# Performance work log

Hardware: AMD Instinct MI355X
Metric: run time of the kernel (lower is better)

The kernel has to match this reference:

```python
import jax, jax.numpy as jnp
import numpy as np

TOL = 1e-3


def _image_grads(F):
    # replicate-pad central difference, matches GradientBatch (conv with [-0.5,0,0.5])
    Fx = jnp.pad(F, ((0, 0), (0, 0), (0, 0), (1, 1)), mode='edge')
    gx = 0.5 * (Fx[:, :, :, 2:] - Fx[:, :, :, :-2])
    Fy = jnp.pad(F, ((0, 0), (0, 0), (1, 1), (0, 0)), mode='edge')
    gy = 0.5 * (Fy[:, :, 2:, :] - Fy[:, :, :-2, :])
    return gx, gy


def _param_to_H(p):
    B = p.shape[0]
    z = jnp.zeros((B, 1, 1), p.dtype)
    return jnp.concatenate([p, z], 1).reshape(B, 3, 3) + jnp.eye(3, dtype=p.dtype)


def _bilinear_sample(A, xw, yw):
    # grid_sample(mode='bilinear', align_corners=True, padding_mode='zeros') at pixel coords (xw, yw)
    B, k, h, w = A.shape
    x0 = jnp.floor(xw)
    y0 = jnp.floor(yw)
    fx = (xw - x0).reshape(B, 1, h * w)
    fy = (yw - y0).reshape(B, 1, h * w)
    Af = A.reshape(B, k, h * w)

    def gather(xi, yi):
        valid = (xi >= 0) & (xi <= w - 1) & (yi >= 0) & (yi <= h - 1)
        xi_c = jnp.clip(xi, 0, w - 1).astype(jnp.int32)
        yi_c = jnp.clip(yi, 0, h - 1).astype(jnp.int32)
        idx = (yi_c * w + xi_c).reshape(B, 1, h * w)
        v = jnp.take_along_axis(Af, jnp.broadcast_to(idx, (B, k, h * w)), axis=2)
        return v * valid.reshape(B, 1, h * w).astype(A.dtype)

    v00 = gather(x0, y0)
    v01 = gather(x0 + 1, y0)
    v10 = gather(x0, y0 + 1)
    v11 = gather(x0 + 1, y0 + 1)
    Q = ((1 - fx) * (1 - fy) * v00 + fx * (1 - fy) * v01
         + (1 - fx) * fy * v10 + fx * fy * v11)
    return Q.reshape(B, k, h, w)


def _deeplk(img, temp, init_param, max_itr):
    B, k, h, w = temp.shape
    dt = temp.dtype
    gx, gy = _image_grads(temp)
    # centered pixel grid (meshgrid in source: x - x.max()/2)
    x = jnp.arange(w, dtype=dt) - (w - 1) / 2.0
    y = jnp.arange(h, dtype=dt) - (h - 1) / 2.0
    X, Y = jnp.meshgrid(x, y)  # (h, w); X varies along w
    Xf = jnp.tile(X.reshape(-1), k)  # [k*h*w], tiled per channel
    Yf = jnp.tile(Y.reshape(-1), k)
    gxf = gx.reshape(B, k * h * w)
    gyf = gy.reshape(B, k * h * w)
    dIdp = jnp.stack([
        Xf * gxf, Yf * gxf, gxf,
        Xf * gyf, Yf * gyf, gyf,
        -Xf * Xf * gxf - Xf * Yf * gyf,
        -Xf * Yf * gxf - Yf * Yf * gyf,
    ], axis=2)  # [B, k*h*w, 8]
    Hmat = jnp.einsum('bnp,bnq->bpq', dIdp, dIdp)  # [B,8,8]
    invH = jnp.linalg.inv(Hmat)
    invH_dIdp = jnp.einsum('bpq,bnq->bpn', invH, dIdp)  # [B,8,k*h*w]
    xy = jnp.stack([X.reshape(-1), Y.reshape(-1), jnp.ones((h * w,), dt)], 0)  # [3, h*w]
    tolf = jnp.asarray(TOL, dt)

    def step(carry, _):
        p, dp = carry
        Hm = _param_to_H(p)
        xyw = jnp.einsum('bij,jn->bin', Hm, xy)  # [B,3,h*w]
        Xw = (xyw[:, 0] / xyw[:, 2]).reshape(B, h, w) + (w - 1) / 2.0
        Yw = (xyw[:, 1] / xyw[:, 2]).reshape(B, h, w) + (h - 1) / 2.0
        Fi_warp = _bilinear_sample(img, Xw, Yw)
        xn = Xw / ((w - 1) / 2.0) - 1.0
        yn = Yw / ((h - 1) / 2.0) - 1.0
        mask = ((xn > -1 + 2.0 / w) & (xn < 1 - 2.0 / w)
                & (yn > -1 + 2.0 / h) & (yn < 1 - 2.0 / h)).astype(dt)
        r = (Fi_warp - temp * mask[:, None]).reshape(B, k * h * w, 1)
        dp_new = jnp.einsum('bpn,bnj->bpj', invH_dIdp, r)  # [B,8,1]
        dp_new = dp_new.at[:, 6:8, 0].set(0.0)  # zero projective terms
        active = (jnp.linalg.norm(dp, axis=1, keepdims=True) > tolf).astype(dt)
        dp2 = active * dp_new  # converged samples freeze (dp stays 0)
        return (p - dp2, dp2), None

    dp0 = jnp.ones((B, 8, 1), dt)
    (p, _), _ = jax.lax.scan(step, (init_param, dp0), None, length=max_itr)
    return p


def setup_inputs() -> dict:
    key = jax.random.key(0)
    k1, k2 = jax.random.split(key)
    B, k, h, w = 8, 8, 256, 256
    img = jax.random.normal(k1, (B, k, h, w), dtype=jnp.float32)
    temp = jax.random.normal(k2, (B, k, h, w), dtype=jnp.float32)
    init_param = jnp.zeros((B, 8, 1), dtype=jnp.float32)
    return {"img": img, "temp": temp, "init_param": init_param, "max_itr": 10}


def reference(img, temp, init_param, max_itr):
    p = _deeplk(img, temp, init_param, max_itr)
    return (p, _param_to_H(p))
```

## Files before the change

kernel.cpp:

```cpp
#include <hip/hip_runtime.h>
#include <hip/hip_bf16.h>

#define B_ 8
#define K_ 8
#define H_ 256
#define W_ 256
#define HW (H_*W_)

__device__ __forceinline__ unsigned short f2bf(float f) {
    __hip_bfloat16 h = __float2bfloat16(f);
    return *reinterpret_cast<unsigned short*>(&h);
}
__device__ __forceinline__ void ub8(uint4 u, float* o) {
    o[0] = __uint_as_float(u.x << 16); o[1] = __uint_as_float(u.x & 0xffff0000u);
    o[2] = __uint_as_float(u.y << 16); o[3] = __uint_as_float(u.y & 0xffff0000u);
    o[4] = __uint_as_float(u.z << 16); o[5] = __uint_as_float(u.z & 0xffff0000u);
    o[6] = __uint_as_float(u.w << 16); o[7] = __uint_as_float(u.w & 0xffff0000u);
}
__device__ __forceinline__ float half_reduce(float v) {
    v += __shfl_down(v, 16, 64);
    v += __shfl_down(v, 8, 64);
    v += __shfl_down(v, 4, 64);
    v += __shfl_down(v, 2, 64);
    v += __shfl_down(v, 1, 64);
    return v;
}
__device__ __forceinline__ float wave_reduce(float v) {
    v += __shfl_down(v, 32, 64);
    v += __shfl_down(v, 16, 64);
    v += __shfl_down(v, 8, 64);
    v += __shfl_down(v, 4, 64);
    v += __shfl_down(v, 2, 64);
    v += __shfl_down(v, 1, 64);
    return v;
}
__device__ __forceinline__ void cstoref(float* p, float v) {
    __hip_atomic_store(p, v, __ATOMIC_RELAXED, __HIP_MEMORY_SCOPE_AGENT);
}
__device__ __forceinline__ float cloadf(const float* p) {
    return __hip_atomic_load((float*)p, __ATOMIC_RELAXED, __HIP_MEMORY_SCOPE_AGENT);
}
__device__ __forceinline__ void cstored(double* p, double v) {
    __hip_atomic_store(p, v, __ATOMIC_RELAXED, __HIP_MEMORY_SCOPE_AGENT);
}
__device__ __forceinline__ double cloadd(const double* p) {
    return __hip_atomic_load((double*)p, __ATOMIC_RELAXED, __HIP_MEMORY_SCOPE_AGENT);
}
__device__ __forceinline__ void cstoreu8(unsigned long long* p, unsigned long long v) {
    __hip_atomic_store(p, v, __ATOMIC_RELAXED, __HIP_MEMORY_SCOPE_AGENT);
}
__device__ __forceinline__ void wait_count(unsigned int* p, unsigned int target) {
    for (int i = 0; i < 1000000; ++i) {
        if (__hip_atomic_load(p, __ATOMIC_RELAXED, __HIP_MEMORY_SCOPE_AGENT) >= target)
            return;
        __builtin_amdgcn_s_sleep(1);
    }
}

__device__ __forceinline__ void pixel_accum(
    const uint4* __restrict__ imgT,
    const uint4 t0, const uint4 g0, const uint4 g1,
    int b, int x, int y,
    float h00, float h01, float h02, float h10, float h11, float h12,
    float h20, float h21, float* aa) {
    const float X = (float)x - 127.5f, Y = (float)y - 127.5f;
    const float zw = h20 * X + h21 * Y + 1.f;
    const float Xw = (h00 * X + h01 * Y + h02) / zw + 127.5f;
    const float Yw = (h10 * X + h11 * Y + h12) / zw + 127.5f;
    const float NLO = -1.f + 2.f / 256.f, NHI = 1.f - 2.f / 256.f;
    const float xn = Xw / 127.5f - 1.f, yn = Yw / 127.5f - 1.f;
    const float m = (xn > NLO && xn < NHI && yn > NLO && yn < NHI) ? 1.f : 0.f;

    const float x0f = floorf(Xw), y0f = floorf(Yw);
    const float fx = Xw - x0f, fy = Yw - y0f;
    const float x1f = x0f + 1.f, y1f = y0f + 1.f;
    const bool vx0 = (x0f >= 0.f) && (x0f <= 255.f);
    const bool vx1 = (x1f >= 0.f) && (x1f <= 255.f);
    const bool vy0 = (y0f >= 0.f) && (y0f <= 255.f);
    const bool vy1 = (y1f >= 0.f) && (y1f <= 255.f);
    const int xi0 = (int)fminf(fmaxf(x0f, 0.f), 255.f);
    const int xi1 = (int)fminf(fmaxf(x1f, 0.f), 255.f);
    const int yi0 = (int)fminf(fmaxf(y0f, 0.f), 255.f);
    const int yi1 = (int)fminf(fmaxf(y1f, 0.f), 255.f);
    const int i00 = yi0 * W_ + xi0, i01 = yi0 * W_ + xi1;
    const int i10 = yi1 * W_ + xi0, i11 = yi1 * W_ + xi1;
    const float w00 = ((vx0 && vy0) ? 1.f : 0.f) * (1.f - fx) * (1.f - fy);
    const float w01 = ((vx1 && vy0) ? 1.f : 0.f) * fx * (1.f - fy);
    const float w10 = ((vx0 && vy1) ? 1.f : 0.f) * (1.f - fx) * fy;
    const float w11 = ((vx1 && vy1) ? 1.f : 0.f) * fx * fy;

    const int base = b * HW;
    const uint4 u00 = imgT[base + i00], u01 = imgT[base + i01];
    const uint4 u10 = imgT[base + i10], u11 = imgT[base + i11];

    float A00[8], A01[8], A10[8], A11[8], GXa[8], GYa[8], TV[8];
    ub8(u00, A00); ub8(u01, A01); ub8(u10, A10); ub8(u11, A11);
    ub8(t0, TV);   ub8(g0, GXa);  ub8(g1, GYa);

    float vx = 0.f, vy = 0.f;
    #pragma unroll
    for (int c = 0; c < 8; ++c) {
        const float Q = w00 * A00[c] + w01 * A01[c] + w10 * A10[c] + w11 * A11[c];
        const float r = Q - TV[c] * m;
        vx += GXa[c] * r;
        vy += GYa[c] * r;
    }
    const float t0a = X * vx, t4a = Y * vy;
    const float cc = t0a + t4a;
    aa[0] += t0a;      aa[1] += Y * vx;  aa[2] += vx;
    aa[3] += X * vy;   aa[4] += t4a;     aa[5] += vy;
    aa[6] -= X * cc;   aa[7] -= Y * cc;
}

__global__ void zero_bar_kernel(unsigned int* __restrict__ bar) {
    bar[threadIdx.x * 32] = 0u;
}

__global__ __launch_bounds__(512, 4) void fused_kernel(
    const float* __restrict__ img, const float* __restrict__ temp,
    uint4* __restrict__ imgT, double* __restrict__ gramP,
    double* __restrict__ invHg, const float* __restrict__ init_param,
    float* __restrict__ sP0, float* __restrict__ sP1,
    unsigned int* __restrict__ bar,
    const int* __restrict__ max_itr, float* __restrict__ out) {
    __shared__ float smem[16384];
    __shared__ float s15s[2][15];
    __shared__ float s8[8];
    __shared__ double sh_invH[64];
    __shared__ double sh_pd[16];
    __shared__ float sh_pf[8];
    __shared__ double gpart[144];
    __shared__ double shA[64], shB[64];

    const int tid = threadIdx.x;
    const int b   = blockIdx.x & 7;
    const int yb  = blockIdx.x >> 3;
    const int h   = tid >> 8;
    const int t2  = tid & 255;
    const int mi_raw = *max_itr;
    const int mi = (mi_raw > 10) ? 10 : mi_raw;

    uint4 rT[2], rGX[2], rGY[2];
    float* region = &smem[h * 8192];
    #pragma unroll
    for (int rl = 0; rl < 2; ++rl) {
        const int row = h + 2 * rl;
        const int y   = yb * 4 + row;
        const int ym = (y > 0) ? y - 1 : 0;
        const int yp = (y < 255) ? y + 1 : 255;
        __syncthreads();
        #pragma unroll
        for (int j = 0; j < 8; ++j) {
            const int slot = t2 + 256 * j;
            const int rowid = slot >> 6, col4 = slot & 63;
            const int c = rowid >> 2, sel = rowid & 3;
            const int sy = (sel == 0) ? ym : ((sel == 2) ? yp : y);
            const float* src = ((sel == 3) ? img : temp)
                             + ((size_t)(b * K_ + c) * HW + sy * W_ + col4 * 4);
            const float4 v = *(const float4*)src;
            *(float4*)&region[(c * 4 + sel) * 256 + col4 * 4] = v;
        }
        __syncthreads();

        const int x = t2;
        const int xm = (x > 0) ? x - 1 : 0;
        const int xp = (x < 255) ? x + 1 : 255;
        float Sxx = 0.f, Sxy = 0.f, Syy = 0.f;
        unsigned int imgp[4] = {0, 0, 0, 0};
        unsigned int tgp[12];
        #pragma unroll
        for (int i = 0; i < 12; ++i) tgp[i] = 0u;
        #pragma unroll
        for (int c = 0; c < 8; ++c) {
            const float* R = &region[c * 1024];
            const float gx = 0.5f * (R[256 + xp] - R[256 + xm]);
            const float gy = 0.5f * (R[512 + x] - R[x]);
            const float tc = R[256 + x];
            const float iv = R[768 + x];
            Sxx += gx * gx; Sxy += gx * gy; Syy += gy * gy;
            const int sh = (c & 1) * 16;
            imgp[c >> 1]     |= ((unsigned int)f2bf(iv)) << sh;
            tgp[c >> 1]      |= ((unsigned int)f2bf(tc)) << sh;
            tgp[4 + (c >> 1)]|= ((unsigned int)f2bf(gx)) << sh;
            tgp[8 + (c >> 1)]|= ((unsigned int)f2bf(gy)) << sh;
        }
        {
            const size_t gpx = (size_t)b * HW + (size_t)y * W_ + x;
            unsigned long long* ip = (unsigned long long*)(imgT + gpx);
            cstoreu8(ip,     ((unsigned long long)imgp[1] << 32) | imgp[0]);
            cstoreu8(ip + 1, ((unsigned long long)imgp[3] << 32) | imgp[2]);
        }
        rT[rl]  = make_uint4(tgp[0], tgp[1], tgp[2],  tgp[3]);
        rGX[rl] = make_uint4(tgp[4], tgp[5], tgp[6],  tgp[7]);
        rGY[rl] = make_uint4(tgp[8], tgp[9], tgp[10], tgp[11]);
        __syncthreads();

        {
            const float X = (float)x - 127.5f;
            const float X2 = X * X;
            const float Xp[5] = {1.f, X, X2, X2 * X, X2 * X2};
            #pragma unroll
            for (int n = 0; n < 5; ++n) {
                region[n * 256 + t2]        = Sxx * Xp[n];
                region[(5 + n) * 256 + t2]  = Sxy * Xp[n];
                region[(10 + n) * 256 + t2] = Syy * Xp[n];
            }
        }
        __syncthreads();
        {
            const int e = t2 >> 5, l = t2 & 31;
            float v = 0.f;
            #pragma unroll
            for (int j = 0; j < 8; ++j) v += region[e * 256 + l + 32 * j];
            v = half_reduce(v);
            if (l == 0) s15s[h][e] = v;
        }
        if (t2 < 224) {
            const int e = 8 + (t2 >> 5), l = t2 & 31;
            float v = 0.f;
            #pragma unroll
            for (int j = 0; j < 8; ++j) v += region[e * 256 + l + 32 * j];
            v = half_reduce(v);
            if (l == 0) s15s[h][e] = v;
        }
        __syncthreads();

        if (t2 < 36) {
            const int aC[8]  = {1, 1, 1, 0, 0, 0, -1, -1};
            const int aNX[8] = {1, 0, 0, 0, 0, 0,  2,  1};
            const int aNY[8] = {0, 1, 0, 0, 0, 0,  0,  1};
            const int bC[8]  = {0, 0, 0, 1, 1, 1, -1, -1};
            const int bNX[8] = {0, 0, 0, 1, 0, 0,  1,  0};
            const int bNY[8] = {0, 0, 0, 0, 1, 0,  1,  2};
            const float* s15 = s15s[h];
            const double Yd = (double)((float)y - 127.5f);
            const double Yp2 = Yd * Yd;
            const double Ypw[5] = {1.0, Yd, Yp2, Yp2 * Yd, Yp2 * Yp2};
            int p = 0, rem = t2;
            while (rem >= 8 - p) { rem -= 8 - p; ++p; }
            const int q = p + rem;
            double g = 0.0;
            const int ac = aC[p] * aC[q];
            if (ac) g += ac * Ypw[aNY[p] + aNY[q]] * (double)s15[aNX[p] + aNX[q]];
            const int ab1 = aC[p] * bC[q];
            if (ab1) g += ab1 * Ypw[aNY[p] + bNY[q]] * (double)s15[5 + aNX[p] + bNX[q]];
            const int ab2 = bC[p] * aC[q];
            if (ab2) g += ab2 * Ypw[bNY[p] + aNY[q]] * (double)s15[5 + bNX[p] + aNX[q]];
            const int bc = bC[p] * bC[q];
            if (bc) g += bc * Ypw[bNY[p] + bNY[q]] * (double)s15[10 + bNX[p] + bNX[q]];
            cstored(&gramP[((size_t)b * 36 + t2) * 256 + y], g);
        }
    }

    asm volatile("s_waitcnt vmcnt(0)" ::: "memory");
    __syncthreads();
    if (tid == 0) {
        __hip_atomic_fetch_add(&bar[(b * 16 + 10) * 32], 1u,
                               __ATOMIC_RELAXED, __HIP_MEMORY_SCOPE_AGENT);
        wait_count(&bar[(b * 16 + 10) * 32], 64u);
    }
    __syncthreads();

    for (int it = 0; it < mi; ++it) {
        if (it > 0) {
            if (tid == 0) {
                wait_count(&bar[(b * 16 + (it - 1)) * 32], 64u);
                if (it == 1) wait_count(&bar[(b * 16 + 11) * 32], 1u);
            }
            __syncthreads();
            if (it == 1 && tid < 64) sh_invH[tid] = cloadd(&invHg[b * 64 + tid]);
            {
                const float* sR = ((it & 1) ? sP0 : sP1) + b * 512;
                const int e = tid >> 6, l = tid & 63;
                float v = cloadf(&sR[e * 64 + l]);
                v = wave_reduce(v);
                if (l == 0) s8[e] = v;
            }
            __syncthreads();
            if (tid < 8) {
                double nrm2 = 0.0;
                #pragma unroll
                for (int k2 = 0; k2 < 8; ++k2) {
                    const double d = sh_pd[8 + k2];
                    nrm2 += d * d;
                }
                double dpn = 0.0;
                if (tid < 6) {
                    #pragma unroll
                    for (int k2 = 0; k2 < 8; ++k2)
                        dpn += sh_invH[tid * 8 + k2] * (double)s8[k2];
                }
                const double dp2 = (sqrt(nrm2) > 1e-3) ? dpn : 0.0;
                const double pnew = sh_pd[tid] - dp2;
                sh_pd[tid]     = pnew;
                sh_pd[8 + tid] = dp2;
            }
            __syncthreads();
        } else {
            if (tid < 8) {
                sh_pd[tid]     = (double)init_param[b * 8 + tid];
                sh_pd[8 + tid] = 1.0;
            }
            __syncthreads();
        }

        const float h00 = 1.f + (float)sh_pd[0], h01 = (float)sh_pd[1], h02 = (float)sh_pd[2];
        const float h10 = (float)sh_pd[3], h11 = 1.f + (float)sh_pd[4], h12 = (float)sh_pd[5];
        const float h20 = (float)sh_pd[6], h21 = (float)sh_pd[7];

        float aa[8];
        #pragma unroll
        for (int e = 0; e < 8; ++e) aa[e] = 0.f;
        #pragma unroll
        for (int sub = 0; sub < 2; ++sub) {
            const int pxl = tid + 512 * sub;
            pixel_accum(imgT, rT[sub], rGX[sub], rGY[sub], b,
                        pxl & 255, yb * 4 + (pxl >> 8),
                        h00, h01, h02, h10, h11, h12, h20, h21, aa);
        }

        float* red = smem;
        #pragma unroll
        for (int e = 0; e < 8; ++e) red[e * 512 + tid] = aa[e];
        __syncthreads();
        {
            const int e = tid >> 6, l = tid & 63;
            float v = 0.f;
            #pragma unroll
            for (int j = 0; j < 8; ++j) v += red[e * 512 + l + 64 * j];
            v = wave_reduce(v);
            if (l == 0) {
                float* sW = (it & 1) ? sP1 : sP0;
                cstoref(&sW[b * 512 + e * 64 + yb], v);
            }
        }

        asm volatile("s_waitcnt vmcnt(0)" ::: "memory");
        __syncthreads();
        if (tid == 0)
            __hip_atomic_fetch_add(&bar[(b * 16 + it) * 32], 1u,
                                   __ATOMIC_RELAXED, __HIP_MEMORY_SCOPE_AGENT);

        if (it == 0 && yb == 0) {
            if (tid < 144) {
                const int e = tid >> 2, q = tid & 3;
                const double* gp = gramP + ((size_t)b * 36 + e) * 256 + q * 64;
                double acc = 0.0;
                #pragma unroll 8
                for (int i = 0; i < 64; ++i) acc += cloadd(&gp[i]);
                gpart[tid] = acc;
            }
            __syncthreads();
            const int i = tid >> 3, j = tid & 7;
            if (tid < 64) {
                const int pp = min(i, j), qq = max(i, j);
                const int tri = 8 * pp - (pp * (pp - 1)) / 2 + (qq - pp);
                shA[tid] = gpart[tri * 4] + gpart[tri * 4 + 1]
                         + gpart[tri * 4 + 2] + gpart[tri * 4 + 3];
                shB[tid] = (i == j) ? 1.0 : 0.0;
            }
            __syncthreads();
            for (int k = 0; k < 8; ++k) {
                const double piv = shA[k * 8 + k];
                __syncthreads();
                if (tid < 64 && i == k) { shA[tid] /= piv; shB[tid] /= piv; }
                __syncthreads();
                double f = 0, ak = 0, bk = 0;
                if (tid < 64) { f = shA[i * 8 + k]; ak = shA[k * 8 + j]; bk = shB[k * 8 + j]; }
                __syncthreads();
                if (tid < 64 && i != k) { shA[tid] -= f * ak; shB[tid] -= f * bk; }
                __syncthreads();
            }
            if (tid < 64) cstored(&invHg[b * 64 + tid], shB[tid]);
            asm volatile("s_waitcnt vmcnt(0)" ::: "memory");
            __syncthreads();
            if (tid == 0)
                __hip_atomic_fetch_add(&bar[(b * 16 + 11) * 32], 1u,
                                       __ATOMIC_RELAXED, __HIP_MEMORY_SCOPE_AGENT);
        }
    }

    if (yb != 0) return;
    if (mi <= 0) {
        if (tid < 8) out[b * 8 + tid] = init_param[b * 8 + tid];
        if (tid < 9) {
            float v = (tid < 8) ? init_param[b * 8 + tid] : 0.f;
            if (tid == 0 || tid == 4 || tid == 8) v += 1.f;
            out[64 + b * 9 + tid] = v;
        }
        return;
    }
    if (tid == 0) wait_count(&bar[(b * 16 + (mi - 1)) * 32], 64u);
    __syncthreads();
    if (mi == 1) {
        if (tid < 64) sh_invH[tid] = cloadd(&invHg[b * 64 + tid]);
    }
    {
        const float* sb = (((mi - 1) & 1) ? sP1 : sP0) + b * 512;
        const int e = tid >> 6, l = tid & 63;
        float v = cloadf(&sb[e * 64 + l]);
        v = wave_reduce(v);
        if (l == 0) s8[e] = v;
    }
    __syncthreads();
    if (tid < 8) {
        double nrm2 = 0.0;
        #pragma unroll
        for (int k2 = 0; k2 < 8; ++k2) {
            const double d = sh_pd[8 + k2];
            nrm2 += d * d;
        }
        double dpn = 0.0;
        if (tid < 6) {
            #pragma unroll
            for (int k2 = 0; k2 < 8; ++k2)
                dpn += sh_invH[tid * 8 + k2] * (double)s8[k2];
        }
        const double dp2 = (sqrt(nrm2) > 1e-3) ? dpn : 0.0;
        const float pf = (float)(sh_pd[tid] - dp2);
        sh_pf[tid] = pf;
        out[b * 8 + tid] = pf;
    }
    __syncthreads();
    if (tid < 9) {
        float v2 = (tid < 8) ? sh_pf[tid] : 0.f;
        if (tid == 0 || tid == 4 || tid == 8) v2 += 1.f;
        out[64 + b * 9 + tid] = v2;
    }
}

extern "C" void kernel_launch(void* const* d_in, const int* in_sizes, int n_in,
                              void* d_out, int out_size, void* d_ws, size_t ws_size,
                              hipStream_t stream) {
    const float* img        = (const float*)d_in[0];
    const float* temp       = (const float*)d_in[1];
    const float* init_param = (const float*)d_in[2];
    const int*   max_itr    = (const int*)d_in[3];
    float* out = (float*)d_out;

    char* w = (char*)d_ws;
    double* gramP = (double*)w;
    double* invHg = gramP + 73728;
    float*  sP0   = (float*)(invHg + 512);
    float*  sP1   = sP0 + 4096;
    unsigned int* bar = (unsigned int*)(sP1 + 4096);
    uint4* imgT   = (uint4*)(w + 1048576);

    zero_bar_kernel<<<1, 128, 0, stream>>>(bar);
    fused_kernel<<<512, 512, 0, stream>>>(img, temp, imgT, gramP, invHg,
                                          init_param, sP0, sP1, bar,
                                          max_itr, out);
}
```

Measured before the change: 192.2 us.

## Split work across 1024 smaller blocks with partitioned barrier counters

Changes the persistent fused kernel from 512 blocks of 512 threads, each covering 4 rows, to 1024 blocks of 256 threads, each covering 2 rows. Each per-iteration grid barrier counter is split into four counters, one per block partition, so atomic contention on a single address is lower; waiters poll the sum of the four. Partial-sum buffers double in size and the reductions change from 64-lane to 32-lane. The aim is better occupancy and less barrier contention. The trade-offs are more blocks to synchronise and four loads per poll, and the spin-wait timeout is cut from 1,000,000 to 20,000 iterations, which could break correctness if blocks are not all co-resident.

```diff
diff --git a/kernel.cpp b/kernel.cpp
--- a/kernel.cpp
+++ b/kernel.cpp
@@ -6,6 +6,8 @@
 #define H_ 256
 #define W_ 256
 #define HW (H_*W_)
+#define NBLK 1024
+#define BPB  128
 
 __device__ __forceinline__ unsigned short f2bf(float f) {
     __hip_bfloat16 h = __float2bfloat16(f);
@@ -25,15 +27,6 @@
     v += __shfl_down(v, 1, 64);
     return v;
 }
-__device__ __forceinline__ float wave_reduce(float v) {
-    v += __shfl_down(v, 32, 64);
-    v += __shfl_down(v, 16, 64);
-    v += __shfl_down(v, 8, 64);
-    v += __shfl_down(v, 4, 64);
-    v += __shfl_down(v, 2, 64);
-    v += __shfl_down(v, 1, 64);
-    return v;
-}
 __device__ __forceinline__ void cstoref(float* p, float v) {
     __hip_atomic_store(p, v, __ATOMIC_RELAXED, __HIP_MEMORY_SCOPE_AGENT);
 }
@@ -49,10 +42,20 @@
 __device__ __forceinline__ void cstoreu8(unsigned long long* p, unsigned long long v) {
     __hip_atomic_store(p, v, __ATOMIC_RELAXED, __HIP_MEMORY_SCOPE_AGENT);
 }
+__device__ __forceinline__ unsigned int cloadu(const unsigned int* p) {
+    return __hip_atomic_load((unsigned int*)p, __ATOMIC_RELAXED, __HIP_MEMORY_SCOPE_AGENT);
+}
 __device__ __forceinline__ void wait_count(unsigned int* p, unsigned int target) {
-    for (int i = 0; i < 1000000; ++i) {
-        if (__hip_atomic_load(p, __ATOMIC_RELAXED, __HIP_MEMORY_SCOPE_AGENT) >= target)
-            return;
+    for (int i = 0; i < 20000; ++i) {
+        if (cloadu(p) >= target) return;
+        __builtin_amdgcn_s_sleep(1);
+    }
+}
+__device__ __forceinline__ void wait_sum4(unsigned int* base, unsigned int target) {
+    for (int i = 0; i < 20000; ++i) {
+        unsigned int s = cloadu(base) + cloadu(base + 32)
+                       + cloadu(base + 64) + cloadu(base + 96);
+        if (s >= target) return;
         __builtin_amdgcn_s_sleep(1);
     }
 }
@@ -116,15 +119,15 @@
     bar[threadIdx.x * 32] = 0u;
 }
 
-__global__ __launch_bounds__(512, 4) void fused_kernel(
+__global__ __launch_bounds__(256, 2) void fused_kernel(
     const float* __restrict__ img, const float* __restrict__ temp,
     uint4* __restrict__ imgT, double* __restrict__ gramP,
     double* __restrict__ invHg, const float* __restrict__ init_param,
     float* __restrict__ sP0, float* __restrict__ sP1,
     unsigned int* __restrict__ bar,
     const int* __restrict__ max_itr, float* __restrict__ out) {
-    __shared__ float smem[16384];
-    __shared__ float s15s[2][15];
+    __shared__ float smem[8192];
+    __shared__ float s15[15];
     __shared__ float s8[8];
     __shared__ double sh_invH[64];
     __shared__ double sh_pd[16];
@@ -135,34 +138,32 @@
     const int tid = threadIdx.x;
     const int b   = blockIdx.x & 7;
     const int yb  = blockIdx.x >> 3;
-    const int h   = tid >> 8;
-    const int t2  = tid & 255;
+    unsigned int* bbar = bar + (size_t)b * 64 * 32;
+    const int part = yb & 3;
     const int mi_raw = *max_itr;
     const int mi = (mi_raw > 10) ? 10 : mi_raw;
 
     uint4 rT[2], rGX[2], rGY[2];
-    float* region = &smem[h * 8192];
-    #pragma unroll
+    #pragma unroll 1
     for (int rl = 0; rl < 2; ++rl) {
-        const int row = h + 2 * rl;
-        const int y   = yb * 4 + row;
+        const int y  = yb * 2 + rl;
         const int ym = (y > 0) ? y - 1 : 0;
         const int yp = (y < 255) ? y + 1 : 255;
         __syncthreads();
         #pragma unroll
         for (int j = 0; j < 8; ++j) {
-            const int slot = t2 + 256 * j;
+            const int slot = tid + 256 * j;
             const int rowid = slot >> 6, col4 = slot & 63;
             const int c = rowid >> 2, sel = rowid & 3;
             const int sy = (sel == 0) ? ym : ((sel == 2) ? yp : y);
             const float* src = ((sel == 3) ? img : temp)
                              + ((size_t)(b * K_ + c) * HW + sy * W_ + col4 * 4);
             const float4 v = *(const float4*)src;
-            *(float4*)&region[(c * 4 + sel) * 256 + col4 * 4] = v;
-        }
-        __syncthreads();
-
-        const int x = t2;
+            *(float4*)&smem[(c * 4 + sel) * 256 + col4 * 4] = v;
+        }
+        __syncthreads();
+
+        const int x = tid;
         const int xm = (x > 0) ? x - 1 : 0;
         const int xp = (x < 255) ? x + 1 : 255;
         float Sxx = 0.f, Sxy = 0.f, Syy = 0.f;
@@ -172,7 +173,7 @@
         for (int i = 0; i < 12; ++i) tgp[i] = 0u;
         #pragma unroll
         for (int c = 0; c < 8; ++c) {
-            const float* R = &region[c * 1024];
+            const float* R = &smem[c * 1024];
             const float gx = 0.5f * (R[256 + xp] - R[256 + xm]);
             const float gy = 0.5f * (R[512 + x] - R[x]);
             const float tc = R[256 + x];
@@ -201,42 +202,41 @@
             const float Xp[5] = {1.f, X, X2, X2 * X, X2 * X2};
             #pragma unroll
             for (int n = 0; n < 5; ++n) {
-                region[n * 256 + t2]        = Sxx * Xp[n];
-                region[(5 + n) * 256 + t2]  = Sxy * Xp[n];
-                region[(10 + n) * 256 + t2] = Syy * Xp[n];
+                smem[n * 256 + tid]        = Sxx * Xp[n];
+                smem[(5 + n) * 256 + tid]  = Sxy * Xp[n];
+                smem[(10 + n) * 256 + tid] = Syy * Xp[n];
             }
         }
         __syncthreads();
         {
-            const int e = t2 >> 5, l = t2 & 31;
+            const int e = tid >> 5, l = tid & 31;
             float v = 0.f;
             #pragma unroll
-            for (int j = 0; j < 8; ++j) v += region[e * 256 + l + 32 * j];
+            for (int j = 0; j < 8; ++j) v += smem[e * 256 + l + 32 * j];
             v = half_reduce(v);
-            if (l == 0) s15s[h][e] = v;
-        }
-        if (t2 < 224) {
-            const int e = 8 + (t2 >> 5), l = t2 & 31;
+            if (l == 0) s15[e] = v;
+        }
+        if (tid < 224) {
+            const int e = 8 + (tid >> 5), l = tid & 31;
             float v = 0.f;
             #pragma unroll
-            for (int j = 0; j < 8; ++j) v += region[e * 256 + l + 32 * j];
+            for (int j = 0; j < 8; ++j) v += smem[e * 256 + l + 32 * j];
             v = half_reduce(v);
-            if (l == 0) s15s[h][e] = v;
-        }
-        __syncthreads();
-
-        if (t2 < 36) {
+            if (l == 0) s15[e] = v;
+        }
+        __syncthreads();
+
+        if (tid < 36) {
             const int aC[8]  = {1, 1, 1, 0, 0, 0, -1, -1};
             const int aNX[8] = {1, 0, 0, 0, 0, 0,  2,  1};
             const int aNY[8] = {0, 1, 0, 0, 0, 0,  0,  1};
             const int bC[8]  = {0, 0, 0, 1, 1, 1, -1, -1};
             const int bNX[8] = {0, 0, 0, 1, 0, 0,  1,  0};
             const int bNY[8] = {0, 0, 0, 0, 1, 0,  1,  2};
-            const float* s15 = s15s[h];
             const double Yd = (double)((float)y - 127.5f);
             const double Yp2 = Yd * Yd;
             const double Ypw[5] = {1.0, Yd, Yp2, Yp2 * Yd, Yp2 * Yp2};
-            int p = 0, rem = t2;
+            int p = 0, rem = tid;
             while (rem >= 8 - p) { rem -= 8 - p; ++p; }
             const int q = p + rem;
             double g = 0.0;
@@ -248,32 +248,33 @@
             if (ab2) g += ab2 * Ypw[bNY[p] + aNY[q]] * (double)s15[5 + bNX[p] + aNX[q]];
             const int bc = bC[p] * bC[q];
             if (bc) g += bc * Ypw[bNY[p] + bNY[q]] * (double)s15[10 + bNX[p] + bNX[q]];
-            cstored(&gramP[((size_t)b * 36 + t2) * 256 + y], g);
+            cstored(&gramP[((size_t)b * 36 + tid) * 256 + y], g);
         }
     }
 
     asm volatile("s_waitcnt vmcnt(0)" ::: "memory");
     __syncthreads();
     if (tid == 0) {
-        __hip_atomic_fetch_add(&bar[(b * 16 + 10) * 32], 1u,
+        __hip_atomic_fetch_add(&bbar[(40 + part) * 32], 1u,
                                __ATOMIC_RELAXED, __HIP_MEMORY_SCOPE_AGENT);
-        wait_count(&bar[(b * 16 + 10) * 32], 64u);
+        wait_sum4(&bbar[40 * 32], 128u);
     }
     __syncthreads();
 
     for (int it = 0; it < mi; ++it) {
         if (it > 0) {
             if (tid == 0) {
-                wait_count(&bar[(b * 16 + (it - 1)) * 32], 64u);
-                if (it == 1) wait_count(&bar[(b * 16 + 11) * 32], 1u);
+                wait_sum4(&bbar[(it - 1) * 4 * 32], 128u);
+                if (it == 1) wait_count(&bbar[44 * 32], 1u);
             }
             __syncthreads();
             if (it == 1 && tid < 64) sh_invH[tid] = cloadd(&invHg[b * 64 + tid]);
             {
-                const float* sR = ((it & 1) ? sP0 : sP1) + b * 512;
-                const int e = tid >> 6, l = tid & 63;
-                float v = cloadf(&sR[e * 64 + l]);
-                v = wave_reduce(v);
+                const float* sR = ((it & 1) ? sP0 : sP1) + b * 1024;
+                const int e = tid >> 5, l = tid & 31;
+                float v = cloadf(&sR[e * 128 + l])      + cloadf(&sR[e * 128 + 32 + l])
+                        + cloadf(&sR[e * 128 + 64 + l]) + cloadf(&sR[e * 128 + 96 + l]);
+                v = half_reduce(v);
                 if (l == 0) s8[e] = v;
             }
             __syncthreads();
@@ -313,32 +314,31 @@
         for (int e = 0; e < 8; ++e) aa[e] = 0.f;
         #pragma unroll
         for (int sub = 0; sub < 2; ++sub) {
-            const int pxl = tid + 512 * sub;
             pixel_accum(imgT, rT[sub], rGX[sub], rGY[sub], b,
-                        pxl & 255, yb * 4 + (pxl >> 8),
+                        tid, yb * 2 + sub,
                         h00, h01, h02, h10, h11, h12, h20, h21, aa);
         }
 
         float* red = smem;
         #pragma unroll
-        for (int e = 0; e < 8; ++e) red[e * 512 + tid] = aa[e];
+        for (int e = 0; e < 8; ++e) red[e * 256 + tid] = aa[e];
         __syncthreads();
         {
-            const int e = tid >> 6, l = tid & 63;
+            const int e = tid >> 5, l = tid & 31;
             float v = 0.f;
             #pragma unroll
-            for (int j = 0; j < 8; ++j) v += red[e * 512 + l + 64 * j];
-            v = wave_reduce(v);
+            for (int j = 0; j < 8; ++j) v += red[e * 256 + l + 32 * j];
+            v = half_reduce(v);
             if (l == 0) {
                 float* sW = (it & 1) ? sP1 : sP0;
-                cstoref(&sW[b * 512 + e * 64 + yb], v);
+                cstoref(&sW[b * 1024 + e * 128 + yb], v);
             }
         }
 
         asm volatile("s_waitcnt vmcnt(0)" ::: "memory");
         __syncthreads();
         if (tid == 0)
-            __hip_atomic_fetch_add(&bar[(b * 16 + it) * 32], 1u,
+            __hip_atomic_fetch_add(&bbar[(it * 4 + part) * 32], 1u,
                                    __ATOMIC_RELAXED, __HIP_MEMORY_SCOPE_AGENT);
 
         if (it == 0 && yb == 0) {
@@ -375,7 +375,7 @@
             asm volatile("s_waitcnt vmcnt(0)" ::: "memory");
             __syncthreads();
             if (tid == 0)
-                __hip_atomic_fetch_add(&bar[(b * 16 + 11) * 32], 1u,
+                __hip_atomic_fetch_add(&bbar[44 * 32], 1u,
                                        __ATOMIC_RELAXED, __HIP_MEMORY_SCOPE_AGENT);
         }
     }
@@ -390,16 +390,15 @@
         }
         return;
     }
-    if (tid == 0) wait_count(&bar[(b * 16 + (mi - 1)) * 32], 64u);
+    if (tid == 0) wait_sum4(&bbar[(mi - 1) * 4 * 32], 128u);
     __syncthreads();
-    if (mi == 1) {
-        if (tid < 64) sh_invH[tid] = cloadd(&invHg[b * 64 + tid]);
-    }
+    if (mi == 1 && tid < 64) sh_invH[tid] = cloadd(&invHg[b * 64 + tid]);
     {
-        const float* sb = (((mi - 1) & 1) ? sP1 : sP0) + b * 512;
-        const int e = tid >> 6, l = tid & 63;
-        float v = cloadf(&sb[e * 64 + l]);
-        v = wave_reduce(v);
+        const float* sb = (((mi - 1) & 1) ? sP1 : sP0) + b * 1024;
+        const int e = tid >> 5, l = tid & 31;
+        float v = cloadf(&sb[e * 128 + l])      + cloadf(&sb[e * 128 + 32 + l])
+                + cloadf(&sb[e * 128 + 64 + l]) + cloadf(&sb[e * 128 + 96 + l]);
+        v = half_reduce(v);
         if (l == 0) s8[e] = v;
     }
     __syncthreads();
@@ -442,12 +441,12 @@
     double* gramP = (double*)w;
     double* invHg = gramP + 73728;
     float*  sP0   = (float*)(invHg + 512);
-    float*  sP1   = sP0 + 4096;
-    unsigned int* bar = (unsigned int*)(sP1 + 4096);
+    float*  sP1   = sP0 + 8192;
+    unsigned int* bar = (unsigned int*)(sP1 + 8192);
     uint4* imgT   = (uint4*)(w + 1048576);
 
-    zero_bar_kernel<<<1, 128, 0, stream>>>(bar);
-    fused_kernel<<<512, 512, 0, stream>>>(img, temp, imgT, gramP, invHg,
-                                          init_param, sP0, sP1, bar,
-                                          max_itr, out);
-}
+    zero_bar_kernel<<<1, 512, 0, stream>>>(bar);
+    fused_kernel<<<NBLK, 256, 0, stream>>>(img, temp, imgT, gramP, invHg,
+                                           init_param, sP0, sP1, bar,
+                                           max_itr, out);
+}
```

Result: slower. 258.6 us (+34.6%).
